# Performance work log

Hardware: AMD Instinct MI355X
Metric: run time of the kernel (lower is better)

Reference implementation:

```python
import jax, jax.numpy as jnp
import numpy as np

DIM = 384
RES = 32
NH = 8
RD = 2
B = 64


def _linear_params(key, out_f, in_f, scale=0.02, bias=True):
    kw, kb = jax.random.split(key)
    W = jax.random.normal(kw, (out_f, in_f), dtype=jnp.float32) * scale
    b = jax.random.normal(kb, (out_f,), dtype=jnp.float32) * scale if bias else None
    return W, b


def setup_inputs() -> dict:
    key = jax.random.key(0)
    ks = jax.random.split(key, 16)
    x = jax.random.normal(ks[0], (B, RES, RES, DIM), dtype=jnp.float32)
    Wc_h, bc_h = _linear_params(ks[1], NH * RD, DIM)
    Wg_h, bg_h = _linear_params(ks[2], RES * RES, RES * RD)
    Wo_h, bo_h = _linear_params(ks[3], DIM, DIM)
    Wc_w, bc_w = _linear_params(ks[4], NH * RD, DIM)
    Wg_w, bg_w = _linear_params(ks[5], RES * RES, RES * RD)
    Wo_w, bo_w = _linear_params(ks[6], DIM, DIM)
    Wmlpc, _ = _linear_params(ks[7], DIM, DIM, bias=False)
    Wr1, br1 = _linear_params(ks[8], DIM // 4, DIM)
    Wr2, br2 = _linear_params(ks[9], DIM * 3, DIM // 4)
    Wp, bp = _linear_params(ks[10], DIM, DIM)
    return dict(x=x, Wc_h=Wc_h, bc_h=bc_h, Wg_h=Wg_h, bg_h=bg_h, Wo_h=Wo_h, bo_h=bo_h,
                Wc_w=Wc_w, bc_w=bc_w, Wg_w=Wg_w, bg_w=bg_w, Wo_w=Wo_w, bo_w=bo_w,
                Wmlpc=Wmlpc, Wr1=Wr1, br1=br1, Wr2=Wr2, br2=br2, Wp=Wp, bp=bp)


def _dynamixer_op(x, Wc, bc, Wg, bg, Wo, bo):
    # x: [N, L, C]
    N, L, C = x.shape
    hd = C // NH
    # compress -> [N, L, NH*RD] -> [N, NH, L*RD]
    w = x @ Wc.T + bc
    w = w.reshape(N, L, NH, RD).transpose(0, 2, 1, 3).reshape(N, NH, L * RD)
    # generate -> [N, NH, L, L], softmax over axis -2 (rows)
    w = (w @ Wg.T + bg).reshape(N, NH, L, L)
    w = jax.nn.softmax(w, axis=-2)
    # x -> [N, NH, hd, L]; mix: y[n,h,d,j] = sum_l x[n,h,d,l] * w[n,h,l,j]
    xh = x.reshape(N, L, NH, hd).transpose(0, 2, 3, 1)
    y = jnp.einsum('nhdl,nhlj->nhdj', xh, w)
    y = y.transpose(0, 3, 1, 2).reshape(N, L, C)
    return y @ Wo.T + bo


def reference(x, Wc_h, bc_h, Wg_h, bg_h, Wo_h, bo_h,
              Wc_w, bc_w, Wg_w, bg_w, Wo_w, bo_w,
              Wmlpc, Wr1, br1, Wr2, br2, Wp, bp):
    Bn, H, W, C = x.shape
    # mix along H: batch over (B, W)
    h = _dynamixer_op(x.transpose(0, 2, 1, 3).reshape(Bn * W, H, C),
                      Wc_h, bc_h, Wg_h, bg_h, Wo_h, bo_h)
    h = h.reshape(Bn, W, H, C).transpose(0, 2, 1, 3)
    # mix along W: batch over (B, H)
    w = _dynamixer_op(x.reshape(Bn * H, W, C),
                      Wc_w, bc_w, Wg_w, bg_w, Wo_w, bo_w)
    w = w.reshape(Bn, H, W, C)
    # channel path (no bias)
    c = x @ Wmlpc.T
    # reweighting: global average pool over H, W
    a = (h + w + c).mean(axis=(1, 2))            # [B, C]
    a = jax.nn.gelu(a @ Wr1.T + br1, approximate=False) @ Wr2.T + br2  # [B, 3C]
    a = a.reshape(Bn, C, 3).transpose(2, 0, 1)   # [3, B, C]
    a = jax.nn.softmax(a, axis=0)[:, :, None, None, :]  # [3, B, 1, 1, C]
    out = h * a[0] + w * a[1] + c * a[2]
    return out @ Wp.T + bp
```

## Files before the change

kernel.cpp:

```cpp
#include <hip/hip_runtime.h>

typedef unsigned short u16;
typedef __bf16 bf16_t;
typedef bf16_t bf16x8 __attribute__((ext_vector_type(8)));
typedef float f32x4 __attribute__((ext_vector_type(4)));

__device__ __forceinline__ u16 f2b(float f) {
  union { float f; unsigned u; } v; v.f = f;
  unsigned r = (v.u + 0x7fffu + ((v.u >> 16) & 1u)) >> 16;
  return (u16)r;
}
__device__ __forceinline__ float b2f(u16 b) {
  union { unsigned u; float f; } v; v.u = ((unsigned)b) << 16;
  return v.f;
}
__device__ __forceinline__ f32x4 mfma16(bf16x8 a, bf16x8 b, f32x4 c) {
  return __builtin_amdgcn_mfma_f32_16x16x32_bf16(a, b, c, 0, 0, 0);
}

struct CvtJobs {
  const float* s[8];
  u16* d[8];
  int n[8];
};
__global__ void k0_cvt(CvtJobs j) {
  int job = blockIdx.y;
  const float* s = j.s[job];
  u16* d = j.d[job];
  int n = j.n[job];
  int stride = gridDim.x * blockDim.x * 4;
  for (int i = (blockIdx.x * blockDim.x + threadIdx.x) * 4; i < n; i += stride) {
    float4 v = *(const float4*)(s + i);
    ushort4 o4;
    o4.x = f2b(v.x); o4.y = f2b(v.y); o4.z = f2b(v.z); o4.w = f2b(v.w);
    *(ushort4*)(d + i) = o4;
  }
}

#define LW 392
#define TW 40
#define AW 40

__global__ __launch_bounds__(256, 2) void k1_mixer(
    const float* __restrict__ x,
    const u16* __restrict__ Wc_h_b, const float* __restrict__ bc_h,
    const u16* __restrict__ Wg_h_b, const float* __restrict__ bg_h,
    const u16* __restrict__ Wc_w_b, const float* __restrict__ bc_w,
    const u16* __restrict__ Wg_w_b, const float* __restrict__ bg_w,
    u16* __restrict__ y_h,
    float* __restrict__ psum_yh, float* __restrict__ psum_yw,
    float* __restrict__ psum_x)
{
  __shared__ u16 xs_b[32 * LW];
  __shared__ u16 xs_t[384 * TW];
  __shared__ u16 attn[8 * 32 * AW];
  __shared__ u16 whead[16 * 72];
  __shared__ float rs[8 * 32];

  const int tid = threadIdx.x;
  const int bid = blockIdx.x;
  const int path = bid >> 11;
  const int n = bid & 2047;
  const int b = n >> 5, o = n & 31;
  long base; int strideL;
  if (path == 0) { base = (long)b * 393216 + (long)o * 384;   strideL = 12288; }
  else           { base = (long)b * 393216 + (long)o * 12288; strideL = 384; }
  const float* xseq = x + base;

  const u16* Wc_b = path ? Wc_w_b : Wc_h_b;
  const float* bc = path ? bc_w : bc_h;
  const u16* Wg_b = path ? Wg_w_b : Wg_h_b;
  const float* bg = path ? bg_w : bg_h;

  for (int i = tid; i < 3072; i += 256) {
    int l = i / 96, c4 = (i % 96) * 4;
    float4 v = *(const float4*)(xseq + (long)l * strideL + c4);
    ushort4 w4;
    w4.x = f2b(v.x); w4.y = f2b(v.y); w4.z = f2b(v.z); w4.w = f2b(v.w);
    *(ushort4*)&xs_b[l * LW + c4] = w4;
  }
  for (int i = tid; i < 576; i += 256) whead[576 + i] = 0;
  __syncthreads();

  if (path == 0) {
    for (int i = tid; i < 3072; i += 256) {
      int c = i % 384, l4 = (i / 384) * 4;
      ushort4 w4;
      w4.x = xs_b[(l4 + 0) * LW + c];
      w4.y = xs_b[(l4 + 1) * LW + c];
      w4.z = xs_b[(l4 + 2) * LW + c];
      w4.w = xs_b[(l4 + 3) * LW + c];
      *(ushort4*)&xs_t[c * TW + l4] = w4;
    }
    for (int c = tid; c < 384; c += 256) {
      float s = 0.f;
      for (int l = 0; l < 32; l++) s += b2f(xs_b[l * LW + c]);
      psum_x[(long)n * 384 + c] = s;
    }
  }

  const int wave = tid >> 6, lane = tid & 63;
  const int lq = lane >> 4, lr = lane & 15;
  const f32x4 z = {0.f, 0.f, 0.f, 0.f};

  if (wave < 2) {
    f32x4 acc = z;
    for (int ks = 0; ks < 12; ks++) {
      bf16x8 af  = *(const bf16x8*)&xs_b[(wave * 16 + lr) * LW + ks * 32 + lq * 8];
      bf16x8 bfr = *(const bf16x8*)(Wc_b + lr * 384 + ks * 32 + lq * 8);
      acc = mfma16(af, bfr, acc);
    }
    float bcv = bc[lr];
    for (int r = 0; r < 4; r++) {
      int l = wave * 16 + lq * 4 + r;
      whead[(lr >> 1) * 72 + l * 2 + (lr & 1)] = f2b(acc[r] + bcv);
    }
  }
  __syncthreads();

  {
    bf16x8 ga0 = *(const bf16x8*)&whead[lr * 72 + lq * 8];
    bf16x8 ga1 = *(const bf16x8*)&whead[lr * 72 + 32 + lq * 8];
    for (int t = 0; t < 16; t++) {
      int nt = wave * 16 + t;
      const u16* wg = Wg_b + (nt * 16 + lr) * 64;
      bf16x8 gb0 = *(const bf16x8*)(wg + lq * 8);
      bf16x8 gb1 = *(const bf16x8*)(wg + 32 + lq * 8);
      f32x4 acc = z;
      acc = mfma16(ga0, gb0, acc);
      acc = mfma16(ga1, gb1, acc);
      if (lq < 2) {
        int m = nt * 16 + lr, ii = m >> 5, jj = m & 31;
        for (int r = 0; r < 4; r++)
          attn[((lq * 4 + r) * 32 + jj) * AW + ii] = f2b(acc[r]);
      }
    }
  }
  __syncthreads();

  {
    int h = tid >> 5, j = tid & 31;
    u16* row = &attn[(h * 32 + j) * AW];
    float v[32]; float mx = -1e30f;
    for (int i = 0; i < 32; i++) {
      v[i] = b2f(row[i]) + bg[i * 32 + j];
      mx = fmaxf(mx, v[i]);
    }
    float s = 0.f;
    for (int i = 0; i < 32; i++) { v[i] = __expf(v[i] - mx); s += v[i]; }
    float inv = 1.0f / s;
    for (int i = 0; i < 32; i++) row[i] = f2b(v[i] * inv);
  }
  __syncthreads();

  if (path == 0) {
    for (int hh = 0; hh < 2; hh++) {
      int h = wave * 2 + hh;
      bf16x8 bf0 = *(const bf16x8*)&attn[(h * 32 + lr) * AW + lq * 8];
      bf16x8 bf1 = *(const bf16x8*)&attn[(h * 32 + 16 + lr) * AW + lq * 8];
      for (int mt = 0; mt < 3; mt++) {
        bf16x8 af = *(const bf16x8*)&xs_t[(h * 48 + mt * 16 + lr) * TW + lq * 8];
        f32x4 a0 = mfma16(af, bf0, z);
        f32x4 a1 = mfma16(af, bf1, z);
        for (int r = 0; r < 4; r++) {
          int c = h * 48 + mt * 16 + lq * 4 + r;
          xs_b[lr * LW + c]        = f2b(a0[r]);
          xs_b[(16 + lr) * LW + c] = f2b(a1[r]);
        }
      }
    }
    __syncthreads();
    u16* yout = y_h + base;
    for (int i = tid; i < 1536; i += 256) {
      int l = i / 48, uu = (i % 48) * 8;
      *(uint4*)(yout + (long)l * strideL + uu) = *(const uint4*)&xs_b[l * LW + uu];
    }
    for (int c = tid; c < 384; c += 256) {
      float s = 0.f;
      for (int jj = 0; jj < 32; jj++) s += b2f(xs_b[jj * LW + c]);
      psum_yh[(long)n * 384 + c] = s;
    }
  } else {
    {
      int h = tid >> 5, l = tid & 31;
      float s = 0.f;
      for (int j = 0; j < 32; j++) s += b2f(attn[(h * 32 + j) * AW + l]);
      rs[h * 32 + l] = s;
    }
    __syncthreads();
    for (int c = tid; c < 384; c += 256) {
      int h = c / 48;
      float s = 0.f;
      for (int l = 0; l < 32; l++) s += b2f(xs_b[l * LW + c]) * rs[h * 32 + l];
      psum_yw[(long)n * 384 + c] = s;
    }
  }
}

__global__ __launch_bounds__(384) void k3_scales(
    const float* __restrict__ psum_yh, const float* __restrict__ psum_yw,
    const float* __restrict__ psum_x,
    const float* __restrict__ Wo_h, const float* __restrict__ bo_h,
    const float* __restrict__ Wo_w, const float* __restrict__ bo_w,
    const float* __restrict__ Wmlpc,
    const float* __restrict__ Wr1, const float* __restrict__ br1,
    const float* __restrict__ Wr2, const float* __restrict__ br2,
    float* __restrict__ scal)
{
  __shared__ float ph[384], pw[384], px[384], a[384], r1[96];
  int b = blockIdx.x, t = threadIdx.x;
  float sh = 0.f, sw = 0.f, sx = 0.f;
  for (int o = 0; o < 32; o++) {
    sh += psum_yh[(long)(b * 32 + o) * 384 + t];
    sw += psum_yw[(long)(b * 32 + o) * 384 + t];
    sx += psum_x[(long)(b * 32 + o) * 384 + t];
  }
  ph[t] = sh; pw[t] = sw; px[t] = sx;
  __syncthreads();
  float s1 = 0.f, s2 = 0.f, s3 = 0.f;
  for (int k = 0; k < 384; k++) {
    s1 += ph[k] * Wo_h[t * 384 + k];
    s2 += pw[k] * Wo_w[t * 384 + k];
    s3 += px[k] * Wmlpc[t * 384 + k];
  }
  a[t] = (s1 + s2 + s3) * (1.f / 1024.f) + bo_h[t] + bo_w[t];
  __syncthreads();
  if (t < 96) {
    float s = 0.f;
    for (int k = 0; k < 384; k++) s += a[k] * Wr1[t * 384 + k];
    s += br1[t];
    r1[t] = s * 0.5f * (1.f + erff(s * 0.70710678118654752f));
  }
  __syncthreads();
  {
    float sv[3];
    for (int si = 0; si < 3; si++) {
      float acc = 0.f;
      for (int k = 0; k < 96; k++) acc += r1[k] * Wr2[(t * 3 + si) * 96 + k];
      sv[si] = acc + br2[t * 3 + si];
    }
    float mx = fmaxf(sv[0], fmaxf(sv[1], sv[2]));
    float e0 = __expf(sv[0] - mx), e1 = __expf(sv[1] - mx), e2 = __expf(sv[2] - mx);
    float inv = 1.f / (e0 + e1 + e2);
    scal[0 * 24576 + b * 384 + t] = e0 * inv;
    scal[1 * 24576 + b * 384 + t] = e1 * inv;
    scal[2 * 24576 + b * 384 + t] = e2 * inv;
  }
}

__device__ __forceinline__ void gemm64(
    const u16* __restrict__ Bglob, const u16* __restrict__ bufA,
    f32x4 acc[2][6], int wm, int wn, int lq, int lr)
{
  const u16* bp0 = Bglob + (wn * 96 + lr) * 384 + lq * 8;
  const u16* ap0 = bufA + (wm * 32 + lr) * 392 + lq * 8;
  bf16x8 bcur[6], af[2];
#pragma unroll
  for (int nt = 0; nt < 6; nt++) bcur[nt] = *(const bf16x8*)(bp0 + nt * 6144);
#pragma unroll
  for (int mt = 0; mt < 2; mt++) af[mt] = *(const bf16x8*)(ap0 + mt * 6272);
  for (int ks = 0; ks < 12; ks++) {
    bf16x8 bnx[6], an[2];
    const int k1 = (ks < 11 ? ks + 1 : 11) * 32;
#pragma unroll
    for (int nt = 0; nt < 6; nt++) bnx[nt] = *(const bf16x8*)(bp0 + nt * 6144 + k1);
#pragma unroll
    for (int mt = 0; mt < 2; mt++) an[mt] = *(const bf16x8*)(ap0 + mt * 6272 + k1);
#pragma unroll
    for (int nt = 0; nt < 6; nt++)
#pragma unroll
      for (int mt = 0; mt < 2; mt++)
        acc[mt][nt] = mfma16(af[mt], bcur[nt], acc[mt][nt]);
#pragma unroll
    for (int nt = 0; nt < 6; nt++) bcur[nt] = bnx[nt];
#pragma unroll
    for (int mt = 0; mt < 2; mt++) af[mt] = an[mt];
  }
}

__global__ __launch_bounds__(512, 4) void k24_final(
    const float* __restrict__ x, const u16* __restrict__ y_h,
    const u16* __restrict__ Wc_w_b, const float* __restrict__ bc_w,
    const u16* __restrict__ Wg_w_b, const float* __restrict__ bg_w,
    const u16* __restrict__ Wo_h_b, const u16* __restrict__ Wo_w_b,
    const u16* __restrict__ Wmlpc_b, const u16* __restrict__ Wp_b,
    const float* __restrict__ bo_h, const float* __restrict__ bo_w,
    const float* __restrict__ bp,
    const float* __restrict__ scal, float* __restrict__ out)
{
  __shared__ u16 bufA[64 * 392];
  __shared__ u16 attn[8 * 32 * AW];
  __shared__ u16 whead[16 * 72];

  const int tid = threadIdx.x;
  const int m0 = blockIdx.x * 64;
  const int b = m0 >> 10;
  const int wave = tid >> 6, lane = tid & 63;
  const int lq = lane >> 4, lr = lane & 15;
  const int wm = wave >> 2, wn = wave & 3;
  const f32x4 z = {0.f, 0.f, 0.f, 0.f};

  for (int i = tid; i < 6144; i += 512) {
    int row = i / 96, c4 = (i % 96) * 4;
    float4 v = *(const float4*)(x + (long)(m0 + row) * 384 + c4);
    ushort4 w4;
    w4.x = f2b(v.x); w4.y = f2b(v.y); w4.z = f2b(v.z); w4.w = f2b(v.w);
    *(ushort4*)&bufA[row * 392 + c4] = w4;
  }
  for (int i = tid; i < 576; i += 512) whead[576 + i] = 0;
  __syncthreads();

  f32x4 acc[2][6];
#pragma unroll
  for (int i = 0; i < 2; i++)
#pragma unroll
    for (int jn = 0; jn < 6; jn++) acc[i][jn] = z;

  gemm64(Wmlpc_b, bufA, acc, wm, wn, lq, lr);
  {
    const float* s2p = scal + 2 * 24576 + b * 384;
    const float* s1p = scal + 1 * 24576 + b * 384;
#pragma unroll
    for (int nt = 0; nt < 6; nt++) {
      int col = wn * 96 + nt * 16 + lr;
      float r = s2p[col] / fmaxf(s1p[col], 1e-30f);
#pragma unroll
      for (int mt = 0; mt < 2; mt++)
#pragma unroll
        for (int rr = 0; rr < 4; rr++) acc[mt][nt][rr] *= r;
    }
  }

  for (int q = 0; q < 2; q++) {
    if (wave < 2) {
      f32x4 ac = z;
      for (int ks = 0; ks < 12; ks++) {
        bf16x8 afg = *(const bf16x8*)&bufA[(q * 32 + wave * 16 + lr) * 392 + ks * 32 + lq * 8];
        bf16x8 bfg = *(const bf16x8*)(Wc_w_b + lr * 384 + ks * 32 + lq * 8);
        ac = mfma16(afg, bfg, ac);
      }
      float bcv = bc_w[lr];
      for (int r = 0; r < 4; r++) {
        int l = wave * 16 + lq * 4 + r;
        whead[(lr >> 1) * 72 + l * 2 + (lr & 1)] = f2b(ac[r] + bcv);
      }
    }
    __syncthreads();
    {
      bf16x8 ga0 = *(const bf16x8*)&whead[lr * 72 + lq * 8];
      bf16x8 ga1 = *(const bf16x8*)&whead[lr * 72 + 32 + lq * 8];
      for (int t = 0; t < 8; t++) {
        int nt = wave * 8 + t;
        const u16* wg = Wg_w_b + (nt * 16 + lr) * 64;
        bf16x8 gb0 = *(const bf16x8*)(wg + lq * 8);
        bf16x8 gb1 = *(const bf16x8*)(wg + 32 + lq * 8);
        f32x4 ac = z;
        ac = mfma16(ga0, gb0, ac);
        ac = mfma16(ga1, gb1, ac);
        if (lq < 2) {
          int m = nt * 16 + lr, ii = m >> 5, jj = m & 31;
          for (int r = 0; r < 4; r++)
            attn[((lq * 4 + r) * 32 + jj) * AW + ii] = f2b(ac[r]);
        }
      }
    }
    __syncthreads();
    if (tid < 256) {
      int h = tid >> 5, j = tid & 31;
      u16* row = &attn[(h * 32 + j) * AW];
      float v[32]; float mx = -1e30f;
      for (int i = 0; i < 32; i++) {
        v[i] = b2f(row[i]) + bg_w[i * 32 + j];
        mx = fmaxf(mx, v[i]);
      }
      float s = 0.f;
      for (int i = 0; i < 32; i++) { v[i] = __expf(v[i] - mx); s += v[i]; }
      float inv = 1.0f / s;
      for (int i = 0; i < 32; i++) row[i] = f2b(v[i] * inv);
    }
    __syncthreads();
    {
      int h = wave;
      bf16x8 bf0 = *(const bf16x8*)&attn[(h * 32 + lr) * AW + lq * 8];
      bf16x8 bf1 = *(const bf16x8*)&attn[(h * 32 + 16 + lr) * AW + lq * 8];
      const float* xg = x + (long)(m0 + q * 32 + lq * 8) * 384;
      for (int mt = 0; mt < 3; mt++) {
        int ca = h * 48 + mt * 16 + lr;
        alignas(16) u16 tmp[8];
#pragma unroll
        for (int e = 0; e < 8; e++) tmp[e] = f2b(xg[(long)e * 384 + ca]);
        bf16x8 afg = *(const bf16x8*)tmp;
        f32x4 a0 = mfma16(afg, bf0, z);
        f32x4 a1 = mfma16(afg, bf1, z);
        for (int r = 0; r < 4; r++) {
          int c = h * 48 + mt * 16 + lq * 4 + r;
          bufA[(q * 32 + lr) * 392 + c]      = f2b(a0[r]);
          bufA[(q * 32 + 16 + lr) * 392 + c] = f2b(a1[r]);
        }
      }
    }
    __syncthreads();
  }

  gemm64(Wo_w_b, bufA, acc, wm, wn, lq, lr);
  {
    const float* s1p = scal + 1 * 24576 + b * 384;
    const float* s0p = scal + 0 * 24576 + b * 384;
#pragma unroll
    for (int nt = 0; nt < 6; nt++) {
      int col = wn * 96 + nt * 16 + lr;
      float r = s1p[col] / fmaxf(s0p[col], 1e-30f);
#pragma unroll
      for (int mt = 0; mt < 2; mt++)
#pragma unroll
        for (int rr = 0; rr < 4; rr++) acc[mt][nt][rr] *= r;
    }
  }
  __syncthreads();

  for (int i = tid; i < 3072; i += 512) {
    int row = i / 48, u8 = (i % 48) * 8;
    *(uint4*)&bufA[row * 392 + u8] = *(const uint4*)(y_h + (long)(m0 + row) * 384 + u8);
  }
  __syncthreads();

  gemm64(Wo_h_b, bufA, acc, wm, wn, lq, lr);
  __syncthreads();

  {
    const float* s0p = scal + 0 * 24576 + b * 384;
    const float* s1p = scal + 1 * 24576 + b * 384;
#pragma unroll
    for (int nt = 0; nt < 6; nt++) {
      int col = wn * 96 + nt * 16 + lr;
      float s0v = s0p[col];
      float bcb = s0v * bo_h[col] + s1p[col] * bo_w[col];
#pragma unroll
      for (int mt = 0; mt < 2; mt++)
#pragma unroll
        for (int r = 0; r < 4; r++) {
          int row = wm * 32 + mt * 16 + lq * 4 + r;
          bufA[row * 392 + col] = f2b(acc[mt][nt][r] * s0v + bcb);
        }
    }
  }
  __syncthreads();

#pragma unroll
  for (int i = 0; i < 2; i++)
#pragma unroll
    for (int jn = 0; jn < 6; jn++) acc[i][jn] = z;
  gemm64(Wp_b, bufA, acc, wm, wn, lq, lr);
#pragma unroll
  for (int nt = 0; nt < 6; nt++) {
    int col = wn * 96 + nt * 16 + lr;
    float bi = bp[col];
#pragma unroll
    for (int mt = 0; mt < 2; mt++)
#pragma unroll
      for (int r = 0; r < 4; r++) {
        int row = m0 + wm * 32 + mt * 16 + lq * 4 + r;
        out[(long)row * 384 + col] = acc[mt][nt][r] + bi;
      }
  }
}

extern "C" void kernel_launch(void* const* d_in, const int* in_sizes, int n_in,
                              void* d_out, int out_size, void* d_ws, size_t ws_size,
                              hipStream_t stream) {
  const float* x     = (const float*)d_in[0];
  const float* Wc_h  = (const float*)d_in[1];
  const float* bc_h  = (const float*)d_in[2];
  const float* Wg_h  = (const float*)d_in[3];
  const float* bg_h  = (const float*)d_in[4];
  const float* Wo_h  = (const float*)d_in[5];
  const float* bo_h  = (const float*)d_in[6];
  const float* Wc_w  = (const float*)d_in[7];
  const float* bc_w  = (const float*)d_in[8];
  const float* Wg_w  = (const float*)d_in[9];
  const float* bg_w  = (const float*)d_in[10];
  const float* Wo_w  = (const float*)d_in[11];
  const float* bo_w  = (const float*)d_in[12];
  const float* Wmlpc = (const float*)d_in[13];
  const float* Wr1   = (const float*)d_in[14];
  const float* br1   = (const float*)d_in[15];
  const float* Wr2   = (const float*)d_in[16];
  const float* br2   = (const float*)d_in[17];
  const float* Wp    = (const float*)d_in[18];
  const float* bp    = (const float*)d_in[19];
  float* out = (float*)d_out;

  char* ws = (char*)d_ws;
  u16* y_h       = (u16*)(ws + 0);
  float* psum_yh = (float*)(ws + 50331648);
  float* psum_yw = (float*)(ws + 53477376);
  float* psum_x  = (float*)(ws + 56623104);
  float* scal    = (float*)(ws + 59768832);
  u16* Wc_h_b    = (u16*)(ws + 60063744);
  u16* Wc_w_b    = (u16*)(ws + 60076032);
  u16* Wg_h_b    = (u16*)(ws + 60088320);
  u16* Wg_w_b    = (u16*)(ws + 60219392);
  u16* Wo_h_b    = (u16*)(ws + 60350464);
  u16* Wo_w_b    = (u16*)(ws + 60645376);
  u16* Wmlpc_b   = (u16*)(ws + 60940288);
  u16* Wp_b      = (u16*)(ws + 61235200);

  CvtJobs jobs;
  jobs.s[0] = Wc_h;  jobs.d[0] = Wc_h_b;  jobs.n[0] = 6144;
  jobs.s[1] = Wc_w;  jobs.d[1] = Wc_w_b;  jobs.n[1] = 6144;
  jobs.s[2] = Wg_h;  jobs.d[2] = Wg_h_b;  jobs.n[2] = 65536;
  jobs.s[3] = Wg_w;  jobs.d[3] = Wg_w_b;  jobs.n[3] = 65536;
  jobs.s[4] = Wo_h;  jobs.d[4] = Wo_h_b;  jobs.n[4] = 147456;
  jobs.s[5] = Wo_w;  jobs.d[5] = Wo_w_b;  jobs.n[5] = 147456;
  jobs.s[6] = Wmlpc; jobs.d[6] = Wmlpc_b; jobs.n[6] = 147456;
  jobs.s[7] = Wp;    jobs.d[7] = Wp_b;    jobs.n[7] = 147456;
  k0_cvt<<<dim3(144, 8), 256, 0, stream>>>(jobs);

  k1_mixer<<<4096, 256, 0, stream>>>(x, Wc_h_b, bc_h, Wg_h_b, bg_h,
      Wc_w_b, bc_w, Wg_w_b, bg_w, y_h, psum_yh, psum_yw, psum_x);

  k3_scales<<<64, 384, 0, stream>>>(psum_yh, psum_yw, psum_x, Wo_h, bo_h,
      Wo_w, bo_w, Wmlpc, Wr1, br1, Wr2, br2, scal);

  k24_final<<<1024, 512, 0, stream>>>(x, y_h, Wc_w_b, bc_w, Wg_w_b, bg_w,
      Wo_h_b, Wo_w_b, Wmlpc_b, Wp_b, bo_h, bo_w, bp, scal, out);
}
```

Baseline: 779.5 us.

## Stage output through LDS, reuse bf16 x tile, and swizzle block order

The final output is first written to shared memory in two 32-row chunks and then stored as coalesced float4 rows, replacing scattered 4-byte global stores. The W-mix A-fragments are now read from the bf16 copy of x already held in shared memory instead of being reloaded with strided fp32 global loads. Block indices are remapped so that consecutive blocks are spread across batches, which changes cache and scheduling locality. This adds extra __syncthreads barriers and reuses the LDS buffer as fp32 scratch.

```diff
diff --git a/kernel.cpp b/kernel.cpp
--- a/kernel.cpp
+++ b/kernel.cpp
@@ -288,12 +288,15 @@
     const float* __restrict__ bp,
     const float* __restrict__ scal, float* __restrict__ out)
 {
-  __shared__ u16 bufA[64 * 392];
+  __shared__ __align__(16) char smem[64 * 392 * 2];
   __shared__ u16 attn[8 * 32 * AW];
   __shared__ u16 whead[16 * 72];
+  u16* bufA = (u16*)smem;
+  float* fbuf = (float*)smem;
 
   const int tid = threadIdx.x;
-  const int m0 = blockIdx.x * 64;
+  const int bid = (blockIdx.x & 7) * 128 + (blockIdx.x >> 3);
+  const int m0 = bid * 64;
   const int b = m0 >> 10;
   const int wave = tid >> 6, lane = tid & 63;
   const int lq = lane >> 4, lr = lane & 15;
@@ -383,15 +386,20 @@
       int h = wave;
       bf16x8 bf0 = *(const bf16x8*)&attn[(h * 32 + lr) * AW + lq * 8];
       bf16x8 bf1 = *(const bf16x8*)&attn[(h * 32 + 16 + lr) * AW + lq * 8];
-      const float* xg = x + (long)(m0 + q * 32 + lq * 8) * 384;
+      bf16x8 afr[3];
+#pragma unroll
       for (int mt = 0; mt < 3; mt++) {
         int ca = h * 48 + mt * 16 + lr;
         alignas(16) u16 tmp[8];
 #pragma unroll
-        for (int e = 0; e < 8; e++) tmp[e] = f2b(xg[(long)e * 384 + ca]);
-        bf16x8 afg = *(const bf16x8*)tmp;
-        f32x4 a0 = mfma16(afg, bf0, z);
-        f32x4 a1 = mfma16(afg, bf1, z);
+        for (int e = 0; e < 8; e++) tmp[e] = bufA[(q * 32 + lq * 8 + e) * 392 + ca];
+        afr[mt] = *(const bf16x8*)tmp;
+      }
+      __syncthreads();
+#pragma unroll
+      for (int mt = 0; mt < 3; mt++) {
+        f32x4 a0 = mfma16(afr[mt], bf0, z);
+        f32x4 a1 = mfma16(afr[mt], bf1, z);
         for (int r = 0; r < 4; r++) {
           int c = h * 48 + mt * 16 + lq * 4 + r;
           bufA[(q * 32 + lr) * 392 + c]      = f2b(a0[r]);
@@ -451,17 +459,30 @@
 #pragma unroll
     for (int jn = 0; jn < 6; jn++) acc[i][jn] = z;
   gemm64(Wp_b, bufA, acc, wm, wn, lq, lr);
-#pragma unroll
-  for (int nt = 0; nt < 6; nt++) {
-    int col = wn * 96 + nt * 16 + lr;
-    float bi = bp[col];
-#pragma unroll
-    for (int mt = 0; mt < 2; mt++)
-#pragma unroll
-      for (int r = 0; r < 4; r++) {
-        int row = m0 + wm * 32 + mt * 16 + lq * 4 + r;
-        out[(long)row * 384 + col] = acc[mt][nt][r] + bi;
-      }
+  __syncthreads();
+
+  for (int chunk = 0; chunk < 2; chunk++) {
+    if (wm == chunk) {
+#pragma unroll
+      for (int nt = 0; nt < 6; nt++) {
+        int col = wn * 96 + nt * 16 + lr;
+        float bi = bp[col];
+#pragma unroll
+        for (int mt = 0; mt < 2; mt++)
+#pragma unroll
+          for (int r = 0; r < 4; r++) {
+            int rowl = mt * 16 + lq * 4 + r;
+            fbuf[rowl * 388 + col] = acc[mt][nt][r] + bi;
+          }
+      }
+    }
+    __syncthreads();
+    for (int i = tid; i < 3072; i += 512) {
+      int rowl = i / 96, c4 = (i % 96) * 4;
+      *(float4*)(out + (long)(m0 + chunk * 32 + rowl) * 384 + c4) =
+          *(const float4*)&fbuf[rowl * 388 + c4];
+    }
+    __syncthreads();
   }
 }
 
```

Result: faster. 756.3 us (-3.0%).
